# Optimization experiments

Measured on AMD Instinct MI355X. Metric: run time of the kernel, lower is better.

## Reference

```python
import jax, jax.numpy as jnp
import numpy as np

B, T, H, U = 32, 2048, 512, 32

def _glorot(key, shape):
    fan_in, fan_out = shape[0], shape[1]
    limit = np.sqrt(6.0 / (fan_in + fan_out))
    return jax.random.uniform(key, shape, jnp.float32, -limit, limit)

def setup_inputs() -> dict:
    key = jax.random.key(0)
    ks = jax.random.split(key, 6)
    return {
        "x": jax.random.normal(ks[0], (B, T, H), jnp.float32),
        "t": jax.random.normal(ks[1], (B, T, H), jnp.float32),
        "kernel_x": _glorot(ks[2], (H, U)),
        "kernel_t": _glorot(ks[3], (H, U)),
        "kernel_a": _glorot(ks[4], (U, H)),
        "bias_x": jnp.zeros((U,), jnp.float32),
        "bias_t": jnp.zeros((U,), jnp.float32),
        "lambd": _glorot(ks[5], (T, 1)),
    }

def reference(x, t, kernel_x, kernel_t, kernel_a, bias_x, bias_t, lambd):
    # gamma, beta: [B, T, U]
    gamma = jnp.tanh(jnp.einsum('bth,hu->btu', x, kernel_x) + bias_x)
    beta = jnp.tanh(jnp.einsum('bth,hu->btu', t, kernel_t) + bias_t)
    # per-timespan convex combination; lambd [T,1] broadcasts over units
    delta = lambd * gamma + (1.0 - lambd) * beta
    # scores [B, T, H]; softmax over the timespan axis (-2)
    scores = jnp.einsum('btu,uh->bth', delta, kernel_a)
    alpha = jax.nn.softmax(scores, axis=-2)
    return alpha
```

## Files before the change

### kernel.cpp

```cpp
#include <hip/hip_runtime.h>
#include <cmath>

#define Hdim 512
#define Udim 32
#define Bdim 32
#define Tdim 2048
#define RM   64
#define KC   32
#define LDX  36
#define CH   128

__global__ __launch_bounds__(256, 3) void k1_gemm_act(
    const float* __restrict__ x, const float* __restrict__ tin,
    const float* __restrict__ kx, const float* __restrict__ kt,
    const float* __restrict__ bx, const float* __restrict__ bt,
    const float* __restrict__ lambd, float* __restrict__ delta)
{
    __shared__ float xs[RM * LDX];
    __shared__ float ts[RM * LDX];
    __shared__ float kxs[KC * Udim];
    __shared__ float kts[KC * Udim];

    const int tid   = threadIdx.x;
    const int u0    = (tid & 7) * 4;
    const int r_thr = tid >> 3;
    const int row0  = blockIdx.x * RM;
    const int lk4   = tid & 7;
    const int lrow  = tid >> 3;

    const float4* xg  = (const float4*)x;
    const float4* tg  = (const float4*)tin;
    const float4* kxg = (const float4*)kx;
    const float4* ktg = (const float4*)kt;

    float4 px[2], pt[2], pwx, pwt;
    float accx[2][4], acct[2][4];
#pragma unroll
    for (int j = 0; j < 2; ++j)
#pragma unroll
        for (int uu = 0; uu < 4; ++uu) { accx[j][uu] = 0.f; acct[j][uu] = 0.f; }

#pragma unroll
    for (int l = 0; l < 2; ++l) {
        const size_t row = (size_t)(row0 + lrow + 32 * l);
        px[l] = xg[row * (Hdim / 4) + lk4];
        pt[l] = tg[row * (Hdim / 4) + lk4];
    }
    pwx = kxg[(size_t)lrow * (Udim / 4) + lk4];
    pwt = ktg[(size_t)lrow * (Udim / 4) + lk4];

#pragma unroll 1
    for (int c = 0; c < Hdim / KC; ++c) {
        __syncthreads();
#pragma unroll
        for (int l = 0; l < 2; ++l) {
            *(float4*)&xs[(lrow + 32 * l) * LDX + lk4 * 4] = px[l];
            *(float4*)&ts[(lrow + 32 * l) * LDX + lk4 * 4] = pt[l];
        }
        *(float4*)&kxs[lrow * Udim + lk4 * 4] = pwx;
        *(float4*)&kts[lrow * Udim + lk4 * 4] = pwt;
        __syncthreads();

        if (c + 1 < Hdim / KC) {
            const int cn = c + 1;
#pragma unroll
            for (int l = 0; l < 2; ++l) {
                const size_t row = (size_t)(row0 + lrow + 32 * l);
                px[l] = xg[row * (Hdim / 4) + cn * (KC / 4) + lk4];
                pt[l] = tg[row * (Hdim / 4) + cn * (KC / 4) + lk4];
            }
            pwx = kxg[(size_t)(cn * KC + lrow) * (Udim / 4) + lk4];
            pwt = ktg[(size_t)(cn * KC + lrow) * (Udim / 4) + lk4];
        }

#pragma unroll
        for (int q = 0; q < KC / 4; ++q) {
            const int k0 = q * 4;
            float wx[4][4], wt[4][4], ax[2][4], at_[2][4];
#pragma unroll
            for (int kk = 0; kk < 4; ++kk) {
                float4 vx = *(const float4*)&kxs[(k0 + kk) * Udim + u0];
                wx[kk][0] = vx.x; wx[kk][1] = vx.y; wx[kk][2] = vx.z; wx[kk][3] = vx.w;
                float4 vt = *(const float4*)&kts[(k0 + kk) * Udim + u0];
                wt[kk][0] = vt.x; wt[kk][1] = vt.y; wt[kk][2] = vt.z; wt[kk][3] = vt.w;
            }
#pragma unroll
            for (int j = 0; j < 2; ++j) {
                float4 va = *(const float4*)&xs[(r_thr + 32 * j) * LDX + k0];
                ax[j][0] = va.x; ax[j][1] = va.y; ax[j][2] = va.z; ax[j][3] = va.w;
                float4 vb = *(const float4*)&ts[(r_thr + 32 * j) * LDX + k0];
                at_[j][0] = vb.x; at_[j][1] = vb.y; at_[j][2] = vb.z; at_[j][3] = vb.w;
            }
#pragma unroll
            for (int j = 0; j < 2; ++j)
#pragma unroll
                for (int kk = 0; kk < 4; ++kk)
#pragma unroll
                    for (int uu = 0; uu < 4; ++uu) {
                        accx[j][uu] = fmaf(ax[j][kk], wx[kk][uu], accx[j][uu]);
                        acct[j][uu] = fmaf(at_[j][kk], wt[kk][uu], acct[j][uu]);
                    }
        }
    }

    float4 bxv = *(const float4*)&bx[u0];
    float4 btv = *(const float4*)&bt[u0];
    float bxa[4] = { bxv.x, bxv.y, bxv.z, bxv.w };
    float bta[4] = { btv.x, btv.y, btv.z, btv.w };

#pragma unroll
    for (int j = 0; j < 2; ++j) {
        const int grow = row0 + r_thr + 32 * j;
        const float lam = lambd[grow & (Tdim - 1)];
        float o[4];
#pragma unroll
        for (int uu = 0; uu < 4; ++uu) {
            float g  = tanhf(accx[j][uu] + bxa[uu]);
            float be = tanhf(acct[j][uu] + bta[uu]);
            o[uu] = lam * g + (1.0f - lam) * be;
        }
        *(float4*)&delta[(size_t)grow * Udim + u0] = make_float4(o[0], o[1], o[2], o[3]);
    }
}

__global__ __launch_bounds__(1024, 2) void k2_softmax(
    const float* __restrict__ delta, const float* __restrict__ ka_g,
    float* __restrict__ alpha)
{
    __shared__ float dsm[2][CH * Udim];
    __shared__ float ms[16][64];
    __shared__ float ls[16][64];

    const int tid = threadIdx.x;
    const int tx  = tid & 63;
    const int ty  = tid >> 6;
    const int b   = blockIdx.x & 31;
    const int ht  = blockIdx.x >> 5;
    const int h   = ht * 64 + tx;

    float ka[Udim];
#pragma unroll
    for (int u = 0; u < Udim; ++u) ka[u] = ka_g[u * Hdim + h];

    const float4* dsrc = (const float4*)(delta + (size_t)b * Tdim * Udim);

    ((float4*)dsm[0])[tid] = dsrc[tid];

    float m = -1e30f, l = 0.f;
#pragma unroll 1
    for (int c = 0; c < Tdim / CH; ++c) {
        __syncthreads();
        const float* cur = dsm[c & 1];
        if (c + 1 < Tdim / CH)
            ((float4*)dsm[(c + 1) & 1])[tid] = dsrc[(size_t)(c + 1) * (CH * Udim / 4) + tid];
#pragma unroll
        for (int i = 0; i < CH / 16; ++i) {
            const int r = ty + 16 * i;
            const float4* dp = (const float4*)(cur + r * Udim);
            float4 q[8];
#pragma unroll
            for (int j = 0; j < 8; ++j) q[j] = dp[j];
            float s0 = 0.f, s1 = 0.f, s2 = 0.f, s3 = 0.f;
#pragma unroll
            for (int j = 0; j < 8; ++j) {
                s0 = fmaf(q[j].x, ka[4 * j],     s0);
                s1 = fmaf(q[j].y, ka[4 * j + 1], s1);
                s2 = fmaf(q[j].z, ka[4 * j + 2], s2);
                s3 = fmaf(q[j].w, ka[4 * j + 3], s3);
            }
            const float s = (s0 + s1) + (s2 + s3);
            const float mn = fmaxf(m, s);
            l = l * __expf(m - mn) + __expf(s - mn);
            m = mn;
        }
    }

    ms[ty][tx] = m;
    ls[ty][tx] = l;
    __syncthreads();
    float M = -1e30f;
#pragma unroll
    for (int w = 0; w < 16; ++w) M = fmaxf(M, ms[w][tx]);
    float L = 0.f;
#pragma unroll
    for (int w = 0; w < 16; ++w) L += ls[w][tx] * __expf(ms[w][tx] - M);
    const float rinv = 1.0f / L;

    ((float4*)dsm[0])[tid] = dsrc[tid];

    float* abase = alpha + (size_t)b * Tdim * Hdim + h;
#pragma unroll 1
    for (int c = 0; c < Tdim / CH; ++c) {
        __syncthreads();
        const float* cur = dsm[c & 1];
        if (c + 1 < Tdim / CH)
            ((float4*)dsm[(c + 1) & 1])[tid] = dsrc[(size_t)(c + 1) * (CH * Udim / 4) + tid];
#pragma unroll
        for (int i = 0; i < CH / 16; ++i) {
            const int r = ty + 16 * i;
            const int t = c * CH + r;
            const float4* dp = (const float4*)(cur + r * Udim);
            float4 q[8];
#pragma unroll
            for (int j = 0; j < 8; ++j) q[j] = dp[j];
            float s0 = 0.f, s1 = 0.f, s2 = 0.f, s3 = 0.f;
#pragma unroll
            for (int j = 0; j < 8; ++j) {
                s0 = fmaf(q[j].x, ka[4 * j],     s0);
                s1 = fmaf(q[j].y, ka[4 * j + 1], s1);
                s2 = fmaf(q[j].z, ka[4 * j + 2], s2);
                s3 = fmaf(q[j].w, ka[4 * j + 3], s3);
            }
            const float s = (s0 + s1) + (s2 + s3);
            abase[(size_t)t * Hdim] = __expf(s - M) * rinv;
        }
    }
}

extern "C" void kernel_launch(void* const* d_in, const int* in_sizes, int n_in,
                              void* d_out, int out_size, void* d_ws, size_t ws_size,
                              hipStream_t stream) {
    const float* x     = (const float*)d_in[0];
    const float* tin   = (const float*)d_in[1];
    const float* kx    = (const float*)d_in[2];
    const float* kt    = (const float*)d_in[3];
    const float* ka    = (const float*)d_in[4];
    const float* bx    = (const float*)d_in[5];
    const float* bt    = (const float*)d_in[6];
    const float* lambd = (const float*)d_in[7];
    float* alpha = (float*)d_out;
    float* delta = (float*)d_ws;

    k1_gemm_act<<<(Bdim * Tdim) / RM, 256, 0, stream>>>(x, tin, kx, kt, bx, bt, lambd, delta);
    k2_softmax<<<256, 1024, 0, stream>>>(delta, ka, alpha);
}
```

Before: 472.0 us.

## Read GEMM weights as wave-uniform scalar loads instead of shared memory tiles

The first kernel's thread mapping changes so that each wavefront owns a group of 8 output units and each lane owns one row. Because the unit offset is wave-uniform (readfirstlane), the weight values can come straight from global memory as scalar loads, removing the shared-memory staging and the LDS reads of the kernel_x and kernel_t tiles. The launch bound goes from 3 to 4 blocks per SM to raise occupancy. The cost is many scalar memory loads per inner step and row-per-lane LDS reads of x and t with stride 36, which may add latency or bank conflicts.

```diff
diff --git a/kernel.cpp b/kernel.cpp
--- a/kernel.cpp
+++ b/kernel.cpp
@@ -8,9 +8,10 @@
 #define RM   64
 #define KC   32
 #define LDX  36
+#define NU   8
 #define CH   128
 
-__global__ __launch_bounds__(256, 3) void k1_gemm_act(
+__global__ __launch_bounds__(256, 4) void k1_gemm_act(
     const float* __restrict__ x, const float* __restrict__ tin,
     const float* __restrict__ kx, const float* __restrict__ kt,
     const float* __restrict__ bx, const float* __restrict__ bt,
@@ -18,109 +19,79 @@
 {
     __shared__ float xs[RM * LDX];
     __shared__ float ts[RM * LDX];
-    __shared__ float kxs[KC * Udim];
-    __shared__ float kts[KC * Udim];
-
-    const int tid   = threadIdx.x;
-    const int u0    = (tid & 7) * 4;
-    const int r_thr = tid >> 3;
-    const int row0  = blockIdx.x * RM;
-    const int lk4   = tid & 7;
-    const int lrow  = tid >> 3;
-
-    const float4* xg  = (const float4*)x;
-    const float4* tg  = (const float4*)tin;
-    const float4* kxg = (const float4*)kx;
-    const float4* ktg = (const float4*)kt;
-
-    float4 px[2], pt[2], pwx, pwt;
-    float accx[2][4], acct[2][4];
-#pragma unroll
-    for (int j = 0; j < 2; ++j)
-#pragma unroll
-        for (int uu = 0; uu < 4; ++uu) { accx[j][uu] = 0.f; acct[j][uu] = 0.f; }
+
+    const int tid  = threadIdx.x;
+    const int lane = tid & 63;
+    const int u0   = __builtin_amdgcn_readfirstlane((tid >> 6) * NU);
+    const int row0 = blockIdx.x * RM;
+
+    const int srow = tid >> 3;
+    const int sf4  = tid & 7;
+
+    const float4* xg = (const float4*)x;
+    const float4* tg = (const float4*)tin;
+
+    float4 px[2], pt[2];
+    float accx[NU], acct[NU];
+#pragma unroll
+    for (int uu = 0; uu < NU; ++uu) { accx[uu] = 0.f; acct[uu] = 0.f; }
 
 #pragma unroll
     for (int l = 0; l < 2; ++l) {
-        const size_t row = (size_t)(row0 + lrow + 32 * l);
-        px[l] = xg[row * (Hdim / 4) + lk4];
-        pt[l] = tg[row * (Hdim / 4) + lk4];
-    }
-    pwx = kxg[(size_t)lrow * (Udim / 4) + lk4];
-    pwt = ktg[(size_t)lrow * (Udim / 4) + lk4];
+        const size_t r = (size_t)(row0 + srow + 32 * l);
+        px[l] = xg[r * (Hdim / 4) + sf4];
+        pt[l] = tg[r * (Hdim / 4) + sf4];
+    }
 
 #pragma unroll 1
     for (int c = 0; c < Hdim / KC; ++c) {
         __syncthreads();
 #pragma unroll
         for (int l = 0; l < 2; ++l) {
-            *(float4*)&xs[(lrow + 32 * l) * LDX + lk4 * 4] = px[l];
-            *(float4*)&ts[(lrow + 32 * l) * LDX + lk4 * 4] = pt[l];
-        }
-        *(float4*)&kxs[lrow * Udim + lk4 * 4] = pwx;
-        *(float4*)&kts[lrow * Udim + lk4 * 4] = pwt;
+            *(float4*)&xs[(srow + 32 * l) * LDX + sf4 * 4] = px[l];
+            *(float4*)&ts[(srow + 32 * l) * LDX + sf4 * 4] = pt[l];
+        }
         __syncthreads();
 
         if (c + 1 < Hdim / KC) {
-            const int cn = c + 1;
 #pragma unroll
             for (int l = 0; l < 2; ++l) {
-                const size_t row = (size_t)(row0 + lrow + 32 * l);
-                px[l] = xg[row * (Hdim / 4) + cn * (KC / 4) + lk4];
-                pt[l] = tg[row * (Hdim / 4) + cn * (KC / 4) + lk4];
+                const size_t r = (size_t)(row0 + srow + 32 * l);
+                px[l] = xg[r * (Hdim / 4) + (c + 1) * (KC / 4) + sf4];
+                pt[l] = tg[r * (Hdim / 4) + (c + 1) * (KC / 4) + sf4];
             }
-            pwx = kxg[(size_t)(cn * KC + lrow) * (Udim / 4) + lk4];
-            pwt = ktg[(size_t)(cn * KC + lrow) * (Udim / 4) + lk4];
         }
 
 #pragma unroll
         for (int q = 0; q < KC / 4; ++q) {
-            const int k0 = q * 4;
-            float wx[4][4], wt[4][4], ax[2][4], at_[2][4];
-#pragma unroll
-            for (int kk = 0; kk < 4; ++kk) {
-                float4 vx = *(const float4*)&kxs[(k0 + kk) * Udim + u0];
-                wx[kk][0] = vx.x; wx[kk][1] = vx.y; wx[kk][2] = vx.z; wx[kk][3] = vx.w;
-                float4 vt = *(const float4*)&kts[(k0 + kk) * Udim + u0];
-                wt[kk][0] = vt.x; wt[kk][1] = vt.y; wt[kk][2] = vt.z; wt[kk][3] = vt.w;
-            }
-#pragma unroll
-            for (int j = 0; j < 2; ++j) {
-                float4 va = *(const float4*)&xs[(r_thr + 32 * j) * LDX + k0];
-                ax[j][0] = va.x; ax[j][1] = va.y; ax[j][2] = va.z; ax[j][3] = va.w;
-                float4 vb = *(const float4*)&ts[(r_thr + 32 * j) * LDX + k0];
-                at_[j][0] = vb.x; at_[j][1] = vb.y; at_[j][2] = vb.z; at_[j][3] = vb.w;
-            }
-#pragma unroll
-            for (int j = 0; j < 2; ++j)
-#pragma unroll
-                for (int kk = 0; kk < 4; ++kk)
-#pragma unroll
-                    for (int uu = 0; uu < 4; ++uu) {
-                        accx[j][uu] = fmaf(ax[j][kk], wx[kk][uu], accx[j][uu]);
-                        acct[j][uu] = fmaf(at_[j][kk], wt[kk][uu], acct[j][uu]);
-                    }
-        }
-    }
-
-    float4 bxv = *(const float4*)&bx[u0];
-    float4 btv = *(const float4*)&bt[u0];
-    float bxa[4] = { bxv.x, bxv.y, bxv.z, bxv.w };
-    float bta[4] = { btv.x, btv.y, btv.z, btv.w };
-
-#pragma unroll
-    for (int j = 0; j < 2; ++j) {
-        const int grow = row0 + r_thr + 32 * j;
-        const float lam = lambd[grow & (Tdim - 1)];
-        float o[4];
-#pragma unroll
-        for (int uu = 0; uu < 4; ++uu) {
-            float g  = tanhf(accx[j][uu] + bxa[uu]);
-            float be = tanhf(acct[j][uu] + bta[uu]);
-            o[uu] = lam * g + (1.0f - lam) * be;
-        }
-        *(float4*)&delta[(size_t)grow * Udim + u0] = make_float4(o[0], o[1], o[2], o[3]);
-    }
+            float4 av = *(const float4*)&xs[lane * LDX + 4 * q];
+            float4 bv = *(const float4*)&ts[lane * LDX + 4 * q];
+            float a4[4] = { av.x, av.y, av.z, av.w };
+            float b4[4] = { bv.x, bv.y, bv.z, bv.w };
+            const float* wxp = kx + (size_t)(c * KC + 4 * q) * Udim + u0;
+            const float* wtp = kt + (size_t)(c * KC + 4 * q) * Udim + u0;
+#pragma unroll
+            for (int kk = 0; kk < 4; ++kk)
+#pragma unroll
+                for (int uu = 0; uu < NU; ++uu) {
+                    accx[uu] = fmaf(a4[kk], wxp[kk * Udim + uu], accx[uu]);
+                    acct[uu] = fmaf(b4[kk], wtp[kk * Udim + uu], acct[uu]);
+                }
+        }
+    }
+
+    const int grow = row0 + lane;
+    const float lam = lambd[grow & (Tdim - 1)];
+    float o[NU];
+#pragma unroll
+    for (int uu = 0; uu < NU; ++uu) {
+        float g  = tanhf(accx[uu] + bx[u0 + uu]);
+        float be = tanhf(acct[uu] + bt[u0 + uu]);
+        o[uu] = lam * g + (1.0f - lam) * be;
+    }
+    float* dp = delta + (size_t)grow * Udim + u0;
+    *(float4*)&dp[0] = make_float4(o[0], o[1], o[2], o[3]);
+    *(float4*)&dp[4] = make_float4(o[4], o[5], o[6], o[7]);
 }
 
 __global__ __launch_bounds__(1024, 2) void k2_softmax(
```

After: 523.3 us. 10.9% more time.

## Load delta rows directly with wave-uniform scalar loads and enlarge k1 row tile

Applied to the files above, without the earlier changes.

The softmax kernel no longer stages delta chunks in shared memory behind block barriers. Each wave reads its row directly from global memory using a wave-uniform index, so the loads can go through the scalar/broadcast path, and the next row is prefetched in registers. The GEMM kernel doubles rows per block to reuse the staged weights more. The risks are higher register pressure in k1 under the 3-waves launch bound and reliance on cache for the repeated delta reads in k2.

```diff
diff --git a/kernel.cpp b/kernel.cpp
--- a/kernel.cpp
+++ b/kernel.cpp
@@ -5,10 +5,10 @@
 #define Udim 32
 #define Bdim 32
 #define Tdim 2048
-#define RM   64
+#define RM   128
 #define KC   32
 #define LDX  36
-#define CH   128
+#define NW   16
 
 __global__ __launch_bounds__(256, 3) void k1_gemm_act(
     const float* __restrict__ x, const float* __restrict__ tin,
@@ -25,58 +25,58 @@
     const int u0    = (tid & 7) * 4;
     const int r_thr = tid >> 3;
     const int row0  = blockIdx.x * RM;
-    const int lk4   = tid & 7;
-    const int lrow  = tid >> 3;
+    const int sf4   = tid & 7;
+    const int srow  = tid >> 3;
 
     const float4* xg  = (const float4*)x;
     const float4* tg  = (const float4*)tin;
     const float4* kxg = (const float4*)kx;
     const float4* ktg = (const float4*)kt;
 
-    float4 px[2], pt[2], pwx, pwt;
-    float accx[2][4], acct[2][4];
-#pragma unroll
-    for (int j = 0; j < 2; ++j)
+    float4 px[4], pt[4], pwx, pwt;
+    float accx[4][4], acct[4][4];
+#pragma unroll
+    for (int j = 0; j < 4; ++j)
 #pragma unroll
         for (int uu = 0; uu < 4; ++uu) { accx[j][uu] = 0.f; acct[j][uu] = 0.f; }
 
 #pragma unroll
-    for (int l = 0; l < 2; ++l) {
-        const size_t row = (size_t)(row0 + lrow + 32 * l);
-        px[l] = xg[row * (Hdim / 4) + lk4];
-        pt[l] = tg[row * (Hdim / 4) + lk4];
-    }
-    pwx = kxg[(size_t)lrow * (Udim / 4) + lk4];
-    pwt = ktg[(size_t)lrow * (Udim / 4) + lk4];
+    for (int l = 0; l < 4; ++l) {
+        const size_t row = (size_t)(row0 + srow + 32 * l);
+        px[l] = xg[row * (Hdim / 4) + sf4];
+        pt[l] = tg[row * (Hdim / 4) + sf4];
+    }
+    pwx = kxg[tid];
+    pwt = ktg[tid];
 
 #pragma unroll 1
     for (int c = 0; c < Hdim / KC; ++c) {
         __syncthreads();
 #pragma unroll
-        for (int l = 0; l < 2; ++l) {
-            *(float4*)&xs[(lrow + 32 * l) * LDX + lk4 * 4] = px[l];
-            *(float4*)&ts[(lrow + 32 * l) * LDX + lk4 * 4] = pt[l];
-        }
-        *(float4*)&kxs[lrow * Udim + lk4 * 4] = pwx;
-        *(float4*)&kts[lrow * Udim + lk4 * 4] = pwt;
+        for (int l = 0; l < 4; ++l) {
+            *(float4*)&xs[(srow + 32 * l) * LDX + sf4 * 4] = px[l];
+            *(float4*)&ts[(srow + 32 * l) * LDX + sf4 * 4] = pt[l];
+        }
+        *(float4*)&kxs[tid * 4] = pwx;
+        *(float4*)&kts[tid * 4] = pwt;
         __syncthreads();
 
         if (c + 1 < Hdim / KC) {
             const int cn = c + 1;
 #pragma unroll
-            for (int l = 0; l < 2; ++l) {
-                const size_t row = (size_t)(row0 + lrow + 32 * l);
-                px[l] = xg[row * (Hdim / 4) + cn * (KC / 4) + lk4];
-                pt[l] = tg[row * (Hdim / 4) + cn * (KC / 4) + lk4];
-            }
-            pwx = kxg[(size_t)(cn * KC + lrow) * (Udim / 4) + lk4];
-            pwt = ktg[(size_t)(cn * KC + lrow) * (Udim / 4) + lk4];
+            for (int l = 0; l < 4; ++l) {
+                const size_t row = (size_t)(row0 + srow + 32 * l);
+                px[l] = xg[row * (Hdim / 4) + cn * (KC / 4) + sf4];
+                pt[l] = tg[row * (Hdim / 4) + cn * (KC / 4) + sf4];
+            }
+            pwx = kxg[cn * (KC * Udim / 4) + tid];
+            pwt = ktg[cn * (KC * Udim / 4) + tid];
         }
 
 #pragma unroll
         for (int q = 0; q < KC / 4; ++q) {
             const int k0 = q * 4;
-            float wx[4][4], wt[4][4], ax[2][4], at_[2][4];
+            float wx[4][4], wt[4][4];
 #pragma unroll
             for (int kk = 0; kk < 4; ++kk) {
                 float4 vx = *(const float4*)&kxs[(k0 + kk) * Udim + u0];
@@ -84,15 +84,16 @@
                 float4 vt = *(const float4*)&kts[(k0 + kk) * Udim + u0];
                 wt[kk][0] = vt.x; wt[kk][1] = vt.y; wt[kk][2] = vt.z; wt[kk][3] = vt.w;
             }
-#pragma unroll
-            for (int j = 0; j < 2; ++j) {
+            float ax[4][4], at_[4][4];
+#pragma unroll
+            for (int j = 0; j < 4; ++j) {
                 float4 va = *(const float4*)&xs[(r_thr + 32 * j) * LDX + k0];
                 ax[j][0] = va.x; ax[j][1] = va.y; ax[j][2] = va.z; ax[j][3] = va.w;
                 float4 vb = *(const float4*)&ts[(r_thr + 32 * j) * LDX + k0];
                 at_[j][0] = vb.x; at_[j][1] = vb.y; at_[j][2] = vb.z; at_[j][3] = vb.w;
             }
 #pragma unroll
-            for (int j = 0; j < 2; ++j)
+            for (int j = 0; j < 4; ++j)
 #pragma unroll
                 for (int kk = 0; kk < 4; ++kk)
 #pragma unroll
@@ -109,7 +110,7 @@
     float bta[4] = { btv.x, btv.y, btv.z, btv.w };
 
 #pragma unroll
-    for (int j = 0; j < 2; ++j) {
+    for (int j = 0; j < 4; ++j) {
         const int grow = row0 + r_thr + 32 * j;
         const float lam = lambd[grow & (Tdim - 1)];
         float o[4];
@@ -123,17 +124,16 @@
     }
 }
 
-__global__ __launch_bounds__(1024, 2) void k2_softmax(
+__global__ __launch_bounds__(1024, 4) void k2_softmax(
     const float* __restrict__ delta, const float* __restrict__ ka_g,
     float* __restrict__ alpha)
 {
-    __shared__ float dsm[2][CH * Udim];
-    __shared__ float ms[16][64];
-    __shared__ float ls[16][64];
+    __shared__ float ms[NW][64];
+    __shared__ float ls[NW][64];
 
     const int tid = threadIdx.x;
     const int tx  = tid & 63;
-    const int ty  = tid >> 6;
+    const int ty  = __builtin_amdgcn_readfirstlane(tid >> 6);
     const int b   = blockIdx.x & 31;
     const int ht  = blockIdx.x >> 5;
     const int h   = ht * 64 + tx;
@@ -142,24 +142,24 @@
 #pragma unroll
     for (int u = 0; u < Udim; ++u) ka[u] = ka_g[u * Hdim + h];
 
-    const float4* dsrc = (const float4*)(delta + (size_t)b * Tdim * Udim);
-
-    ((float4*)dsm[0])[tid] = dsrc[tid];
+    const float* dbase = delta + (size_t)b * Tdim * Udim;
 
     float m = -1e30f, l = 0.f;
-#pragma unroll 1
-    for (int c = 0; c < Tdim / CH; ++c) {
-        __syncthreads();
-        const float* cur = dsm[c & 1];
-        if (c + 1 < Tdim / CH)
-            ((float4*)dsm[(c + 1) & 1])[tid] = dsrc[(size_t)(c + 1) * (CH * Udim / 4) + tid];
-#pragma unroll
-        for (int i = 0; i < CH / 16; ++i) {
-            const int r = ty + 16 * i;
-            const float4* dp = (const float4*)(cur + r * Udim);
-            float4 q[8];
-#pragma unroll
-            for (int j = 0; j < 8; ++j) q[j] = dp[j];
+    {
+        float4 q[8];
+        {
+            const float4* p = (const float4*)(dbase + (size_t)ty * Udim);
+#pragma unroll
+            for (int j = 0; j < 8; ++j) q[j] = p[j];
+        }
+#pragma unroll 2
+        for (int i = 0; i < Tdim / NW; ++i) {
+            const int rn = ty + 16 * ((i + 1) & (Tdim / NW - 1));
+            const float4* np = (const float4*)(dbase + (size_t)rn * Udim);
+            float4 nq[8];
+#pragma unroll
+            for (int j = 0; j < 8; ++j) nq[j] = np[j];
+
             float s0 = 0.f, s1 = 0.f, s2 = 0.f, s3 = 0.f;
 #pragma unroll
             for (int j = 0; j < 8; ++j) {
@@ -172,6 +172,8 @@
             const float mn = fmaxf(m, s);
             l = l * __expf(m - mn) + __expf(s - mn);
             m = mn;
+#pragma unroll
+            for (int j = 0; j < 8; ++j) q[j] = nq[j];
         }
     }
 
@@ -180,29 +182,28 @@
     __syncthreads();
     float M = -1e30f;
 #pragma unroll
-    for (int w = 0; w < 16; ++w) M = fmaxf(M, ms[w][tx]);
+    for (int w = 0; w < NW; ++w) M = fmaxf(M, ms[w][tx]);
     float L = 0.f;
 #pragma unroll
-    for (int w = 0; w < 16; ++w) L += ls[w][tx] * __expf(ms[w][tx] - M);
+    for (int w = 0; w < NW; ++w) L += ls[w][tx] * __expf(ms[w][tx] - M);
     const float rinv = 1.0f / L;
 
-    ((float4*)dsm[0])[tid] = dsrc[tid];
-
     float* abase = alpha + (size_t)b * Tdim * Hdim + h;
-#pragma unroll 1
-    for (int c = 0; c < Tdim / CH; ++c) {
-        __syncthreads();
-        const float* cur = dsm[c & 1];
-        if (c + 1 < Tdim / CH)
-            ((float4*)dsm[(c + 1) & 1])[tid] = dsrc[(size_t)(c + 1) * (CH * Udim / 4) + tid];
-#pragma unroll
-        for (int i = 0; i < CH / 16; ++i) {
-            const int r = ty + 16 * i;
-            const int t = c * CH + r;
-            const float4* dp = (const float4*)(cur + r * Udim);
-            float4 q[8];
-#pragma unroll
-            for (int j = 0; j < 8; ++j) q[j] = dp[j];
+    {
+        float4 q[8];
+        {
+            const float4* p = (const float4*)(dbase + (size_t)ty * Udim);
+#pragma unroll
+            for (int j = 0; j < 8; ++j) q[j] = p[j];
+        }
+#pragma unroll 2
+        for (int i = 0; i < Tdim / NW; ++i) {
+            const int rn = ty + 16 * ((i + 1) & (Tdim / NW - 1));
+            const float4* np = (const float4*)(dbase + (size_t)rn * Udim);
+            float4 nq[8];
+#pragma unroll
+            for (int j = 0; j < 8; ++j) nq[j] = np[j];
+
             float s0 = 0.f, s1 = 0.f, s2 = 0.f, s3 = 0.f;
 #pragma unroll
             for (int j = 0; j < 8; ++j) {
@@ -212,7 +213,10 @@
                 s3 = fmaf(q[j].w, ka[4 * j + 3], s3);
             }
             const float s = (s0 + s1) + (s2 + s3);
+            const int t = ty + 16 * i;
             abase[(size_t)t * Hdim] = __expf(s - M) * rinv;
+#pragma unroll
+            for (int j = 0; j < 8; ++j) q[j] = nq[j];
         }
     }
 }
```

Result: slower. 558.7 us (+18.4%).
